# Optimization experiments

Measured on AMD Instinct MI355X. Metric: run time of the kernel, lower is better.

The kernel has to match this reference:

```python
import jax, jax.numpy as jnp
import numpy as np

B, S, D, H = 4, 2048, 1024, 16
DEPTH = D // H
NEG = float(-2**32 + 1)


def setup_inputs() -> dict:
    key = jax.random.key(0)
    ks = jax.random.split(key, 9)
    std = 1.0 / np.sqrt(D)
    return {
        "q": jax.random.normal(ks[0], (B, S, D), jnp.float32),
        "k": jax.random.normal(ks[1], (B, S, D), jnp.float32),
        "v": jax.random.normal(ks[2], (B, S, D), jnp.float32),
        "Wq": jax.random.normal(ks[3], (D, D), jnp.float32) * std,
        "bq": jnp.zeros((D,), jnp.float32),
        "Wk": jax.random.normal(ks[4], (D, D), jnp.float32) * std,
        "bk": jnp.zeros((D,), jnp.float32),
        "Wv": jax.random.normal(ks[5], (D, D), jnp.float32) * std,
        "bv": jnp.zeros((D,), jnp.float32),
    }


def _split_heads(x):
    # (B,S,D) -> head-major (H*B, S, depth), matching tf stack-on-axis0
    return x.reshape(B, S, H, DEPTH).transpose(2, 0, 1, 3).reshape(H * B, S, DEPTH)


def _merge_heads(x):
    # (H*B, S, depth) -> (B, S, D), heads concatenated on feature dim
    return x.reshape(H, B, S, DEPTH).transpose(1, 2, 0, 3).reshape(B, S, D)


def _attention(qh, kh, vh):
    scale = 1.0 / jnp.sqrt(jnp.float32(DEPTH))
    scores = jnp.einsum("nsd,ntd->nst", qh, kh) * scale  # (N,S,S)
    key_mask = jnp.sign(jnp.abs(jnp.sum(kh, axis=-1)))    # (N,S)
    scores = jnp.where(key_mask[:, None, :] == 0, NEG, scores)
    tril = jnp.tril(jnp.ones((S, S), jnp.float32))
    scores = jnp.where(tril[None] == 0, NEG, scores)
    attn = jax.nn.softmax(scores, axis=-1)
    query_mask = jnp.sign(jnp.abs(jnp.sum(qh, axis=-1)))   # (N,S)
    attn = attn * query_mask[:, :, None]
    return jnp.einsum("nst,ntd->nsd", attn, vh)


def reference(q, k, v, Wq, bq, Wk, bk, Wv, bv):
    qh = _split_heads(q @ Wq + bq)
    kh = _split_heads(k @ Wk + bk)
    vh = _split_heads(v @ Wv + bv)
    out = _attention(qh, kh, vh)
    return _merge_heads(out)
```

## Files before the change

kernel.cpp:

```cpp
#include <hip/hip_runtime.h>

#define S_LEN   2048
#define D_MODEL 1024
#define NB      4
#define NH      16
#define DEP     64
#define NHEADS  64
#define M_ROWS  8192

typedef __bf16 bf16_t;
typedef bf16_t bf16x8 __attribute__((ext_vector_type(8)));
typedef bf16_t bf16x2 __attribute__((ext_vector_type(2)));
typedef float  f32x4  __attribute__((ext_vector_type(4)));
typedef float  f32x16 __attribute__((ext_vector_type(16)));
typedef unsigned int u32x4 __attribute__((ext_vector_type(4)));

#define LOG2E 1.4426950408889634f
#define QSCALE 0.18033688011112043f

#if __has_builtin(__builtin_amdgcn_exp2f)
  #define EXP2(x) __builtin_amdgcn_exp2f(x)
#else
  #define EXP2(x) exp2f(x)
#endif

#define GLOBAL_AS(p) ((const __attribute__((address_space(1))) void*)(p))
#define LDS_AS(p)    ((__attribute__((address_space(3))) void*)(p))

__device__ __forceinline__ unsigned short bf16r(float f) {
  unsigned u = __builtin_bit_cast(unsigned, f);
  u = (u + 0x7FFFu + ((u >> 16) & 1u)) >> 16;
  return (unsigned short)u;
}

__device__ __forceinline__ unsigned pkbf(float lo, float hi) {
  bf16x2 t;
  t[0] = (bf16_t)lo;
  t[1] = (bf16_t)hi;
  return __builtin_bit_cast(unsigned, t);
}

__device__ __forceinline__ bf16x8 exppack8(
    float a0, float a1, float a2, float a3,
    float a4, float a5, float a6, float a7, float& ssum) {
  float e0 = EXP2(a0);
  float e1 = EXP2(a1);
  float e2 = EXP2(a2);
  float e3 = EXP2(a3);
  float e4 = EXP2(a4);
  float e5 = EXP2(a5);
  float e6 = EXP2(a6);
  float e7 = EXP2(a7);
  ssum += ((e0 + e1) + (e2 + e3)) + ((e4 + e5) + (e6 + e7));
  u32x4 fw = {pkbf(e0, e1), pkbf(e2, e3), pkbf(e4, e5), pkbf(e6, e7)};
  return __builtin_bit_cast(bf16x8, fw);
}

__global__ __launch_bounds__(256) void transpose_cvt_w3(
    const float* __restrict__ Wq, const float* __restrict__ Wk,
    const float* __restrict__ Wv,
    unsigned short* __restrict__ oq, unsigned short* __restrict__ ok,
    unsigned short* __restrict__ ov) {
  __shared__ unsigned short tile[32][33];
  int z = blockIdx.z;
  const float* in = (z == 0) ? Wq : (z == 1) ? Wk : Wv;
  unsigned short* out = (z == 0) ? oq : (z == 1) ? ok : ov;
  int bx = blockIdx.x * 32;
  int by = blockIdx.y * 32;
  int tx = threadIdx.x & 31, ty = threadIdx.x >> 5;
  for (int i = ty; i < 32; i += 8)
    tile[i][tx] = bf16r(in[(by + i) * D_MODEL + bx + tx]);
  __syncthreads();
  for (int i = ty; i < 32; i += 8)
    out[(size_t)(bx + i) * D_MODEL + by + tx] = tile[tx][i];
}

__global__ __launch_bounds__(256, 3) void gemm_qkv3(
    const float* __restrict__ Aq, const float* __restrict__ Ak,
    const float* __restrict__ Av,
    const unsigned short* __restrict__ Btq, const unsigned short* __restrict__ Btk,
    const unsigned short* __restrict__ Btv,
    const float* __restrict__ bq, const float* __restrict__ bk,
    const float* __restrict__ bv,
    unsigned short* __restrict__ oq, unsigned short* __restrict__ ok,
    unsigned short* __restrict__ ov) {
  __shared__ __align__(16) float          Asb[128 * 64];
  __shared__ __align__(16) unsigned short Bsb[128 * 64];
  int z = blockIdx.z;
  const float* A           = (z == 0) ? Aq  : (z == 1) ? Ak  : Av;
  const unsigned short* Bt = (z == 0) ? Btq : (z == 1) ? Btk : Btv;
  const float* bias        = (z == 0) ? bq  : (z == 1) ? bk  : bv;
  unsigned short* out      = (z == 0) ? oq  : (z == 1) ? ok  : ov;
  const float scale        = (z == 0) ? QSCALE : 1.0f;
  int tid = threadIdx.x, lane = tid & 63, wid = tid >> 6;
  int lr = lane & 15, lg = lane >> 4;
  int m0 = blockIdx.x * 128, n0 = blockIdx.y * 128;
  int wr = wid >> 1, wc = wid & 1;
  f32x4 acc[4][4] = {};
  for (int kt = 0; kt < D_MODEL / 64; kt++) {
    int k0 = kt * 64;
    if (kt) __syncthreads();
#pragma unroll
    for (int i = 0; i < 8; i++) {
      int chunk = i * 256 + tid;
      int row = chunk >> 4, c = chunk & 15;
      int csrc = c ^ (row & 7);
      __builtin_amdgcn_global_load_lds(
          GLOBAL_AS(A + (size_t)(m0 + row) * D_MODEL + k0 + csrc * 4),
          LDS_AS(Asb + (size_t)(i * 256 + wid * 64) * 4), 16, 0, 0);
    }
#pragma unroll
    for (int i = 0; i < 4; i++) {
      int chunk = i * 256 + tid;
      int r = chunk >> 3, c = chunk & 7;
      int csrc = c ^ (r & 7);
      __builtin_amdgcn_global_load_lds(
          GLOBAL_AS(Bt + (size_t)(n0 + r) * D_MODEL + k0 + csrc * 8),
          LDS_AS(Bsb + (size_t)(i * 256 + wid * 64) * 8), 16, 0, 0);
    }
    __syncthreads();
#pragma unroll
    for (int ks = 0; ks < 2; ks++) {
      bf16x8 af[4], bfr[4];
#pragma unroll
      for (int mi = 0; mi < 4; mi++) {
        int row = wr * 64 + mi * 16 + lr;
        int c0 = (ks * 8 + lg * 2) ^ (row & 7);
        int c1 = (ks * 8 + lg * 2 + 1) ^ (row & 7);
        f32x4 a0 = *(const f32x4*)(Asb + row * 64 + c0 * 4);
        f32x4 a1 = *(const f32x4*)(Asb + row * 64 + c1 * 4);
        u32x4 w = {pkbf(a0[0], a0[1]), pkbf(a0[2], a0[3]),
                   pkbf(a1[0], a1[1]), pkbf(a1[2], a1[3])};
        af[mi] = __builtin_bit_cast(bf16x8, w);
      }
#pragma unroll
      for (int ni = 0; ni < 4; ni++) {
        int row = wc * 64 + ni * 16 + lr;
        int c = (ks * 4 + lg) ^ (row & 7);
        bfr[ni] = *(const bf16x8*)(Bsb + row * 64 + c * 8);
      }
#pragma unroll
      for (int mi = 0; mi < 4; mi++)
#pragma unroll
        for (int ni = 0; ni < 4; ni++)
          acc[mi][ni] = __builtin_amdgcn_mfma_f32_16x16x32_bf16(
              af[mi], bfr[ni], acc[mi][ni], 0, 0, 0);
    }
  }
  if (z != 2) {
#pragma unroll
    for (int mi = 0; mi < 4; mi++) {
#pragma unroll
      for (int ni = 0; ni < 4; ni++) {
        int col = n0 + wc * 64 + ni * 16 + lr;
        float bvv = bias[col];
        int h = col >> 6, d = col & 63;
#pragma unroll
        for (int r = 0; r < 4; r++) {
          int row = m0 + wr * 64 + mi * 16 + lg * 4 + r;
          int b = row >> 11, s = row & (S_LEN - 1);
          float val = (acc[mi][ni][r] + bvv) * scale;
          out[((size_t)(h * NB + b) * S_LEN + s) * DEP + d] = bf16r(val);
        }
      }
    }
  } else {
    int sadj_off = (lg == 1) ? 4 : (lg == 2) ? -4 : 0;
#pragma unroll
    for (int mi = 0; mi < 4; mi++) {
#pragma unroll
      for (int ni = 0; ni < 4; ni++) {
        int col = n0 + wc * 64 + ni * 16 + lr;
        float bvv = bias[col];
        int row0 = m0 + wr * 64 + mi * 16 + lg * 4;
        int b = row0 >> 11, s = (row0 & (S_LEN - 1)) + sadj_off;
        ushort4 w;
        w.x = bf16r(acc[mi][ni][0] + bvv);
        w.y = bf16r(acc[mi][ni][1] + bvv);
        w.z = bf16r(acc[mi][ni][2] + bvv);
        w.w = bf16r(acc[mi][ni][3] + bvv);
        *(ushort4*)(out + ((size_t)((col >> 6) * NB + b) * DEP + (col & 63)) * S_LEN + s) = w;
      }
    }
  }
}

__global__ __launch_bounds__(256, 2) void attn_fwd(
    const unsigned short* __restrict__ Q,
    const unsigned short* __restrict__ K,
    const unsigned short* __restrict__ Vt,
    float* __restrict__ out) {
  __shared__ __align__(16) char smem[65536];
  const int tid = threadIdx.x, lane = tid & 63, wid = tid >> 6;
  const int l31 = lane & 31, hi = lane >> 5;
  const int id = blockIdx.x;
  const int xcd = id & 7, hh = (id >> 3) & 7, u = id >> 6;
  const int n = xcd * 8 + hh;
  const int h = n >> 2, b = n & 3;
  const unsigned short* Qh = Q + (size_t)n * S_LEN * DEP;
  const unsigned short* Kh = K + (size_t)n * S_LEN * DEP;
  const unsigned short* Vh = Vt + (size_t)n * DEP * S_LEN;
  const int S31 = (l31 & 7) << 4;
  const int scol = ((lane & 7) ^ (lane >> 3)) * 8;
  const int srow = lane >> 3;

#define STAGE_TILE(kvb, bi)                                                   \
  {                                                                           \
    char* base_ = smem + (bi) * 16384;                                        \
    const unsigned short* ksrc =                                              \
        Kh + (size_t)((kvb) + wid * 16 + srow) * DEP + scol;                  \
    const unsigned short* vsrc =                                              \
        Vh + (size_t)(wid * 16 + srow) * S_LEN + (kvb) + scol;                \
    unsigned short* kdst = (unsigned short*)base_ + wid * 16 * 64;            \
    unsigned short* vdst = (unsigned short*)(base_ + 8192) + wid * 16 * 64;   \
    __builtin_amdgcn_global_load_lds(GLOBAL_AS(ksrc), LDS_AS(kdst), 16, 0, 0);\
    __builtin_amdgcn_global_load_lds(GLOBAL_AS(ksrc + 8 * DEP),               \
                                     LDS_AS(kdst + 8 * 64), 16, 0, 0);        \
    __builtin_amdgcn_global_load_lds(GLOBAL_AS(vsrc), LDS_AS(vdst), 16, 0, 0);\
    __builtin_amdgcn_global_load_lds(GLOBAL_AS(vsrc + 8 * S_LEN),             \
                                     LDS_AS(vdst + 8 * 64), 16, 0, 0);        \
  }

#define DO_HALF(KROW, VKS, qfv, o0v, o1v, ssumv, qrowv, domask)               \
  {                                                                           \
    f32x16 p = {};                                                            \
    __builtin_amdgcn_s_setprio(1);                                            \
    _Pragma("unroll")                                                         \
    for (int ds = 0; ds < 4; ds++) {                                          \
      int off = (ds * 32 + hi * 16) ^ S31;                                    \
      bf16x8 kf = *(const bf16x8*)(kb + (l31 + (KROW)) * 128 + off);          \
      p = __builtin_amdgcn_mfma_f32_32x32x16_bf16(kf, qfv[ds], p, 0, 0, 0);   \
    }                                                                         \
    __builtin_amdgcn_s_setprio(0);                                            \
    if (domask) {                                                             \
      _Pragma("unroll")                                                       \
      for (int r = 0; r < 16; r++) {                                          \
        int kvr = kvb + (KROW) + (r & 3) + 8 * (r >> 2) + 4 * hi;             \
        if (kvr > (qrowv)) p[r] = -3.0e38f;                                   \
      }                                                                       \
    }                                                                         \
    bf16x8 paA_ = exppack8(p[0], p[1], p[2], p[3],                            \
                           p[4], p[5], p[6], p[7], ssumv);                    \
    bf16x8 paB_ = exppack8(p[8], p[9], p[10], p[11],                          \
                           p[12], p[13], p[14], p[15], ssumv);                \
    __builtin_amdgcn_s_setprio(1);                                            \
    {                                                                         \
      int off0 = ((VKS) * 32 + hi * 16) ^ S31;                                \
      int off1 = (((VKS) + 1) * 32 + hi * 16) ^ S31;                          \
      bf16x8 vfa = *(const bf16x8*)(vb + l31 * 128 + off0);                   \
      bf16x8 vfb = *(const bf16x8*)(vb + (l31 + 32) * 128 + off0);            \
      o0v = __builtin_amdgcn_mfma_f32_32x32x16_bf16(vfa, paA_, o0v, 0, 0, 0); \
      o1v = __builtin_amdgcn_mfma_f32_32x32x16_bf16(vfb, paA_, o1v, 0, 0, 0); \
      bf16x8 vfc = *(const bf16x8*)(vb + l31 * 128 + off1);                   \
      bf16x8 vfd = *(const bf16x8*)(vb + (l31 + 32) * 128 + off1);            \
      o0v = __builtin_amdgcn_mfma_f32_32x32x16_bf16(vfc, paB_, o0v, 0, 0, 0); \
      o1v = __builtin_amdgcn_mfma_f32_32x32x16_bf16(vfd, paB_, o1v, 0, 0, 0); \
    }                                                                         \
    __builtin_amdgcn_s_setprio(0);                                            \
  }

#define EPILOGUE(o0v, o1v, lv, q0v)                                           \
  {                                                                           \
    const float inv = 1.0f / (lv);                                            \
    float* ow = (float*)(smem + wid * 8192);                                  \
    const int es = (l31 & 7) << 2;                                            \
    _Pragma("unroll")                                                         \
    for (int r = 0; r < 16; r++) {                                            \
      int d0 = (r & 3) + 8 * (r >> 2) + 4 * hi;                               \
      ow[l31 * 64 + (d0 ^ es)]        = o0v[r] * inv;                         \
      ow[l31 * 64 + ((d0 + 32) ^ es)] = o1v[r] * inv;                         \
    }                                                                         \
    asm volatile("s_waitcnt lgkmcnt(0)" ::: "memory");                        \
    __builtin_amdgcn_sched_barrier(0);                                        \
    _Pragma("unroll")                                                         \
    for (int i = 0; i < 8; i++) {                                             \
      int idx = i * 64 + lane;                                                \
      int row = idx >> 4;                                                     \
      int c4 = idx & 15;                                                      \
      float4 vv = *(const float4*)&ow[row * 64 + ((c4 * 4) ^ ((row & 7) << 2))]; \
      *(float4*)(out + (size_t)(b * S_LEN + (q0v) + row) * D_MODEL + h * DEP + c4 * 4) = vv; \
    }                                                                         \
  }

  for (int pass = 0; pass < 2; ++pass) {
    const int m = pass ? 31 - (u * 4 + wid) : u * 4 + wid;
    const int nt_w = m + 1;
    const int nt_blk = pass ? 32 - 4 * u : 4 * u + 4;
    const int q0 = m * 64;
    const int qrowA = q0 + l31;
    const int qrowB = q0 + 32 + l31;

    bf16x8 qfA[4], qfB[4];
#pragma unroll
    for (int ds = 0; ds < 4; ds++) {
      qfA[ds] = *(const bf16x8*)(Qh + (size_t)qrowA * DEP + ds * 16 + hi * 8);
      qfB[ds] = *(const bf16x8*)(Qh + (size_t)qrowB * DEP + ds * 16 + hi * 8);
    }

    f32x16 oA0 = {}, oA1 = {}, oB0 = {}, oB1 = {};
    float lA = 0.f, lB = 0.f;

    __syncthreads();
    STAGE_TILE(0, 0);
    STAGE_TILE(64, 1);

    for (int t = 0; t < nt_blk; ++t) {
      if (t + 2 < nt_blk) {
        STAGE_TILE((t + 2) * 64, (t + 2) & 3);
        asm volatile("s_waitcnt vmcnt(8)" ::: "memory");
      } else if (t + 1 < nt_blk) {
        asm volatile("s_waitcnt vmcnt(4)" ::: "memory");
      } else {
        asm volatile("s_waitcnt vmcnt(0)" ::: "memory");
      }
      __builtin_amdgcn_s_barrier();
      asm volatile("" ::: "memory");
      if (t < nt_w) {
        const char* kb = smem + (t & 3) * 16384;
        const char* vb = kb + 8192;
        const int kvb = t * 64;
        const bool diag = (t == nt_w - 1);
        float ssumA = 0.f, ssumB = 0.f;

        DO_HALF(0, 0, qfA, oA0, oA1, ssumA, qrowA, diag);
        DO_HALF(0, 0, qfB, oB0, oB1, ssumB, qrowB, 0);
        if (!diag) {
          DO_HALF(32, 2, qfA, oA0, oA1, ssumA, qrowA, 0);
        }
        DO_HALF(32, 2, qfB, oB0, oB1, ssumB, qrowB, diag);

        ssumA += __shfl_xor(ssumA, 32);
        lA += ssumA;
        ssumB += __shfl_xor(ssumB, 32);
        lB += ssumB;
      }
    }
    __syncthreads();

    EPILOGUE(oA0, oA1, lA, q0);
    asm volatile("s_waitcnt lgkmcnt(0)" ::: "memory");
    EPILOGUE(oB0, oB1, lB, q0 + 32);
  }
#undef STAGE_TILE
#undef DO_HALF
#undef EPILOGUE
}

extern "C" void kernel_launch(void* const* d_in, const int* in_sizes, int n_in,
                              void* d_out, int out_size, void* d_ws, size_t ws_size,
                              hipStream_t stream) {
  const float* q  = (const float*)d_in[0];
  const float* k  = (const float*)d_in[1];
  const float* v  = (const float*)d_in[2];
  const float* Wq = (const float*)d_in[3];
  const float* bq = (const float*)d_in[4];
  const float* Wk = (const float*)d_in[5];
  const float* bk = (const float*)d_in[6];
  const float* Wv = (const float*)d_in[7];
  const float* bv = (const float*)d_in[8];
  float* out = (float*)d_out;

  const size_t WN = (size_t)D_MODEL * D_MODEL;
  const size_t HN = (size_t)NHEADS * S_LEN * DEP;

  unsigned short* Qh  = (unsigned short*)d_ws;
  unsigned short* Kh  = Qh + HN;
  unsigned short* Vts = Kh + HN;
  unsigned short* Wqt = Vts + HN;
  unsigned short* Wkt = Wqt + WN;
  unsigned short* Wvt = Wkt + WN;

  transpose_cvt_w3<<<dim3(32, 32, 3), 256, 0, stream>>>(Wq, Wk, Wv, Wqt, Wkt, Wvt);

  gemm_qkv3<<<dim3(M_ROWS / 128, D_MODEL / 128, 3), 256, 0, stream>>>(
      q, k, v, Wqt, Wkt, Wvt, bq, bk, bv, Qh, Kh, Vts);

  attn_fwd<<<512, 256, 0, stream>>>(Qh, Kh, Vts, out);
}
```

Before: 167.6 us.

## Stage 128-wide KV tiles with double buffering instead of 64-wide triple prefetch

KV staging now copies 128 keys per stage into two 32KB LDS buffers, where it previously used four 16KB buffers with a two-tile-ahead prefetch. Each stage is processed as two 64-key sub-tiles. The change halves the number of barriers and waitcnt points per pass, which cuts synchronisation overhead. In exchange the prefetch runs only one stage ahead and waits on vmcnt(0) each iteration, which may expose more memory latency.

Measured after the change: 168.2 us. About the same (+0.4%).

```diff
diff --git a/kernel.cpp b/kernel.cpp
--- a/kernel.cpp
+++ b/kernel.cpp
@@ -204,21 +204,29 @@
   const int scol = ((lane & 7) ^ (lane >> 3)) * 8;
   const int srow = lane >> 3;
 
-#define STAGE_TILE(kvb, bi)                                                   \
+#define STAGE_T128(kvb, bi)                                                   \
   {                                                                           \
-    char* base_ = smem + (bi) * 16384;                                        \
-    const unsigned short* ksrc =                                              \
-        Kh + (size_t)((kvb) + wid * 16 + srow) * DEP + scol;                  \
-    const unsigned short* vsrc =                                              \
-        Vh + (size_t)(wid * 16 + srow) * S_LEN + (kvb) + scol;                \
-    unsigned short* kdst = (unsigned short*)base_ + wid * 16 * 64;            \
-    unsigned short* vdst = (unsigned short*)(base_ + 8192) + wid * 16 * 64;   \
-    __builtin_amdgcn_global_load_lds(GLOBAL_AS(ksrc), LDS_AS(kdst), 16, 0, 0);\
-    __builtin_amdgcn_global_load_lds(GLOBAL_AS(ksrc + 8 * DEP),               \
-                                     LDS_AS(kdst + 8 * 64), 16, 0, 0);        \
-    __builtin_amdgcn_global_load_lds(GLOBAL_AS(vsrc), LDS_AS(vdst), 16, 0, 0);\
-    __builtin_amdgcn_global_load_lds(GLOBAL_AS(vsrc + 8 * S_LEN),             \
-                                     LDS_AS(vdst + 8 * 64), 16, 0, 0);        \
+    char* base_ = smem + (bi) * 32768;                                        \
+    unsigned short* kdst = (unsigned short*)base_;                            \
+    unsigned short* vdst0 = (unsigned short*)(base_ + 16384);                 \
+    unsigned short* vdst1 = (unsigned short*)(base_ + 24576);                 \
+    _Pragma("unroll")                                                         \
+    for (int i_ = 0; i_ < 4; i_++) {                                          \
+      int r_ = wid * 32 + i_ * 8;                                             \
+      __builtin_amdgcn_global_load_lds(                                       \
+          GLOBAL_AS(Kh + (size_t)((kvb) + r_ + srow) * DEP + scol),           \
+          LDS_AS(kdst + (size_t)r_ * 64), 16, 0, 0);                          \
+    }                                                                         \
+    _Pragma("unroll")                                                         \
+    for (int i_ = 0; i_ < 2; i_++) {                                          \
+      int d_ = wid * 16 + i_ * 8;                                             \
+      __builtin_amdgcn_global_load_lds(                                       \
+          GLOBAL_AS(Vh + (size_t)(d_ + srow) * S_LEN + (kvb) + scol),         \
+          LDS_AS(vdst0 + (size_t)d_ * 64), 16, 0, 0);                         \
+      __builtin_amdgcn_global_load_lds(                                       \
+          GLOBAL_AS(Vh + (size_t)(d_ + srow) * S_LEN + (kvb) + 64 + scol),    \
+          LDS_AS(vdst1 + (size_t)d_ * 64), 16, 0, 0);                         \
+    }                                                                         \
   }
 
 #define DO_HALF(KROW, VKS, qfv, o0v, o1v, ssumv, qrowv, domask)               \
@@ -235,7 +243,7 @@
     if (domask) {                                                             \
       _Pragma("unroll")                                                       \
       for (int r = 0; r < 16; r++) {                                          \
-        int kvr = kvb + (KROW) + (r & 3) + 8 * (r >> 2) + 4 * hi;             \
+        int kvr = kvb64 + (KROW) + (r & 3) + 8 * (r >> 2) + 4 * hi;           \
         if (kvr > (qrowv)) p[r] = -3.0e38f;                                   \
       }                                                                       \
     }                                                                         \
@@ -284,8 +292,7 @@
 
   for (int pass = 0; pass < 2; ++pass) {
     const int m = pass ? 31 - (u * 4 + wid) : u * 4 + wid;
-    const int nt_w = m + 1;
-    const int nt_blk = pass ? 32 - 4 * u : 4 * u + 4;
+    const int ntT = pass ? 16 - 2 * u : 2 * u + 2;
     const int q0 = m * 64;
     const int qrowA = q0 + l31;
     const int qrowB = q0 + 32 + l31;
@@ -301,25 +308,23 @@
     float lA = 0.f, lB = 0.f;
 
     __syncthreads();
-    STAGE_TILE(0, 0);
-    STAGE_TILE(64, 1);
-
-    for (int t = 0; t < nt_blk; ++t) {
-      if (t + 2 < nt_blk) {
-        STAGE_TILE((t + 2) * 64, (t + 2) & 3);
-        asm volatile("s_waitcnt vmcnt(8)" ::: "memory");
-      } else if (t + 1 < nt_blk) {
-        asm volatile("s_waitcnt vmcnt(4)" ::: "memory");
-      } else {
-        asm volatile("s_waitcnt vmcnt(0)" ::: "memory");
-      }
+    STAGE_T128(0, 0);
+
+    for (int T = 0; T < ntT; ++T) {
+      asm volatile("s_waitcnt vmcnt(0)" ::: "memory");
       __builtin_amdgcn_s_barrier();
       asm volatile("" ::: "memory");
-      if (t < nt_w) {
-        const char* kb = smem + (t & 3) * 16384;
-        const char* vb = kb + 8192;
-        const int kvb = t * 64;
-        const bool diag = (t == nt_w - 1);
+      if (T + 1 < ntT) STAGE_T128((T + 1) * 128, (T + 1) & 1);
+      const char* Kb = smem + (T & 1) * 32768;
+      const char* Vb = Kb + 16384;
+#pragma unroll
+      for (int h2 = 0; h2 < 2; ++h2) {
+        const int t64 = 2 * T + h2;
+        if (t64 > m) break;
+        const char* kb = Kb + h2 * 8192;
+        const char* vb = Vb + h2 * 8192;
+        const int kvb64 = t64 * 64;
+        const bool diag = (t64 == m);
         float ssumA = 0.f, ssumB = 0.f;
 
         DO_HALF(0, 0, qfA, oA0, oA1, ssumA, qrowA, diag);
@@ -341,7 +346,7 @@
     asm volatile("s_waitcnt lgkmcnt(0)" ::: "memory");
     EPILOGUE(oB0, oB1, lB, q0 + 32);
   }
-#undef STAGE_TILE
+#undef STAGE_T128
 #undef DO_HALF
 #undef EPILOGUE
 }
```
